# Kernel tuning notes

Measured on AMD Instinct MI355X. Metric: run time of the kernel, lower is better.

Reference implementation:

```python
import jax, jax.numpy as jnp
import numpy as np
import math

D_MODEL = 512
NUM_HEADS = 8
B, S = 2, 4096


def setup_inputs() -> dict:
    key = jax.random.key(0)
    ks = jax.random.split(key, 11)
    d = D_MODEL
    sc = 1.0 / math.sqrt(d)
    return {
        "query": jax.random.normal(ks[0], (B, S, d), jnp.float32),
        "key": jax.random.normal(ks[1], (B, S, d), jnp.float32),
        "value": jax.random.normal(ks[2], (B, S, d), jnp.float32),
        "Wq": jax.random.normal(ks[3], (d, d), jnp.float32) * sc,
        "bq": jnp.zeros((d,), jnp.float32),
        "Wk": jax.random.normal(ks[4], (d, d), jnp.float32) * sc,
        "bk": jnp.zeros((d,), jnp.float32),
        "Wv": jax.random.normal(ks[5], (d, d), jnp.float32) * sc,
        "bv": jnp.zeros((d,), jnp.float32),
        "Wo": jax.random.normal(ks[6], (d, d), jnp.float32) * sc,
        "bo": jnp.zeros((d,), jnp.float32),
    }


def reference(query, key, value, Wq, bq, Wk, bk, Wv, bv, Wo, bo):
    b, q_len, d_model = query.shape
    k_len = key.shape[1]
    h = NUM_HEADS
    d_k = d_model // h
    q = (query @ Wq.T + bq).reshape(b, q_len, h, d_k)
    k = (key @ Wk.T + bk).reshape(b, k_len, h, d_k)
    v = (value @ Wv.T + bv).reshape(b, k_len, h, d_k)
    # NOTE: faithful to source — softmax WITHOUT pre-scaling, then divide by sqrt(d_k)
    comp = jnp.einsum('bqhd,bkhd->bhqk', q, k)
    attn = jax.nn.softmax(comp, axis=-1) / jnp.sqrt(jnp.asarray(d_k, comp.dtype))
    x = jnp.einsum('bhqk,bkhd->bqhd', attn, v)
    return x.reshape(b, q_len, d_model) @ Wo.T + bo
```

## Files before the change

### kernel.cpp

```cpp
#include <hip/hip_runtime.h>

typedef _Float16 f16;
typedef __fp16 fp16x2 __attribute__((ext_vector_type(2)));
typedef _Float16 half4 __attribute__((ext_vector_type(4)));
typedef _Float16 half8 __attribute__((ext_vector_type(8)));
typedef float f32x4 __attribute__((ext_vector_type(4)));
typedef float float4v __attribute__((ext_vector_type(4)));
typedef float float2v __attribute__((ext_vector_type(2)));

#define LOG2E 1.44269504088896340736f

__device__ __forceinline__ half8 cat8(half4 a, half4 b) {
    half8 r;
    r[0] = a[0]; r[1] = a[1]; r[2] = a[2]; r[3] = a[3];
    r[4] = b[0]; r[5] = b[1]; r[6] = b[2]; r[7] = b[3];
    return r;
}

union H8 { fp16x2 h2[4]; half8 h8; };

#define TR8(baddr, d0,d1,d2,d3,d4,d5,d6,d7)                                   \
  asm volatile("ds_read_b64_tr_b16 %0, %8 offset:0\n\t"                       \
               "ds_read_b64_tr_b16 %1, %8 offset:512\n\t"                     \
               "ds_read_b64_tr_b16 %2, %8 offset:128\n\t"                     \
               "ds_read_b64_tr_b16 %3, %8 offset:640\n\t"                     \
               "ds_read_b64_tr_b16 %4, %8 offset:256\n\t"                     \
               "ds_read_b64_tr_b16 %5, %8 offset:768\n\t"                     \
               "ds_read_b64_tr_b16 %6, %8 offset:384\n\t"                     \
               "ds_read_b64_tr_b16 %7, %8 offset:896"                         \
               : "=&v"(d0),"=&v"(d1),"=&v"(d2),"=&v"(d3),                     \
                 "=&v"(d4),"=&v"(d5),"=&v"(d6),"=&v"(d7)                      \
               : "v"(baddr) : "memory")

#define LGKM0_FENCE()                                                          \
  do { asm volatile("s_waitcnt lgkmcnt(0)" ::: "memory");                      \
       __builtin_amdgcn_sched_barrier(0); } while (0)

__device__ __forceinline__ float rowmax16(const f32x4 sf[4]) {
    float a = fmaxf(fmaxf(sf[0][0], sf[0][1]), fmaxf(sf[0][2], sf[0][3]));
    float b = fmaxf(fmaxf(sf[1][0], sf[1][1]), fmaxf(sf[1][2], sf[1][3]));
    float c = fmaxf(fmaxf(sf[2][0], sf[2][1]), fmaxf(sf[2][2], sf[2][3]));
    float d = fmaxf(fmaxf(sf[3][0], sf[3][1]), fmaxf(sf[3][2], sf[3][3]));
    return fmaxf(fmaxf(a, b), fmaxf(c, d));
}

__device__ __forceinline__ void max_defer(
    const f32x4 sf[4], float& mL, f32x4 o[4], f32x4& la)
{
    float vm = rowmax16(sf);
    vm = fmaxf(vm, __shfl_xor(vm, 16, 64));
    vm = fmaxf(vm, __shfl_xor(vm, 32, 64));
    float vmL = vm * LOG2E;
    if (__any(vmL > mL + 8.0f)) {
        float mn = fmaxf(mL, vmL);
        float al = __builtin_amdgcn_exp2f(mL - mn);
        la *= al;
        #pragma unroll
        for (int db = 0; db < 4; ++db) o[db] *= al;
        mL = mn;
    }
}

__device__ __forceinline__ void exp_pack(
    const f32x4 sf[4], float mL, H8& pb0, H8& pb1)
{
    float pe[16];
    #pragma unroll
    for (int kb = 0; kb < 4; ++kb)
        #pragma unroll
        for (int ro = 0; ro < 4; ++ro)
            pe[kb * 4 + ro] = __builtin_amdgcn_exp2f(fmaf(sf[kb][ro], LOG2E, -mL));
    pb0.h2[0] = __builtin_amdgcn_cvt_pkrtz(pe[0],  pe[1]);
    pb0.h2[1] = __builtin_amdgcn_cvt_pkrtz(pe[2],  pe[3]);
    pb0.h2[2] = __builtin_amdgcn_cvt_pkrtz(pe[4],  pe[5]);
    pb0.h2[3] = __builtin_amdgcn_cvt_pkrtz(pe[6],  pe[7]);
    pb1.h2[0] = __builtin_amdgcn_cvt_pkrtz(pe[8],  pe[9]);
    pb1.h2[1] = __builtin_amdgcn_cvt_pkrtz(pe[10], pe[11]);
    pb1.h2[2] = __builtin_amdgcn_cvt_pkrtz(pe[12], pe[13]);
    pb1.h2[3] = __builtin_amdgcn_cvt_pkrtz(pe[14], pe[15]);
}

__global__ __launch_bounds__(256) void qkv_proj(
    const float* __restrict__ Aq, const float* __restrict__ Ak, const float* __restrict__ Av,
    const float* __restrict__ Wq, const float* __restrict__ Wk, const float* __restrict__ Wv,
    const float* __restrict__ bq, const float* __restrict__ bk, const float* __restrict__ bv,
    f16* __restrict__ Qh, f16* __restrict__ Kh, f16* __restrict__ Vh)
{
    const int z = blockIdx.z;
    const float* __restrict__ A    = (z == 0) ? Aq : (z == 1) ? Ak : Av;
    const float* __restrict__ W    = (z == 0) ? Wq : (z == 1) ? Wk : Wv;
    const float* __restrict__ bias = (z == 0) ? bq : (z == 1) ? bk : bv;
    f16* __restrict__ dst          = (z == 0) ? Qh : (z == 1) ? Kh : Vh;

    __shared__ __align__(16) f16 As[128 * 40];
    __shared__ __align__(16) f16 Ws[128 * 40];

    const int t  = threadIdx.x;
    const int m0 = blockIdx.y * 128;
    const int n0 = blockIdx.x * 128;
    const int w = t >> 6, lane = t & 63, lr = lane & 15, lg = lane >> 4;
    const int wr = w >> 1, wc = w & 1;

    f32x4 acc[4][4] = {};

    for (int k0 = 0; k0 < 512; k0 += 32) {
        #pragma unroll
        for (int it = 0; it < 2; ++it) {
            int c = t + it * 256;
            int row  = c >> 2;
            int col8 = (c & 3) * 8;

            const float* ga = A + (size_t)(m0 + row) * 512 + k0 + col8;
            float4v a0 = *(const float4v*)ga;
            float4v a1 = *(const float4v*)(ga + 4);
            half8 ha;
            ha[0] = (f16)a0[0]; ha[1] = (f16)a0[1]; ha[2] = (f16)a0[2]; ha[3] = (f16)a0[3];
            ha[4] = (f16)a1[0]; ha[5] = (f16)a1[1]; ha[6] = (f16)a1[2]; ha[7] = (f16)a1[3];
            *(half8*)&As[row * 40 + col8] = ha;

            const float* gw = W + (size_t)(n0 + row) * 512 + k0 + col8;
            float4v w0 = *(const float4v*)gw;
            float4v w1 = *(const float4v*)(gw + 4);
            half8 hw;
            hw[0] = (f16)w0[0]; hw[1] = (f16)w0[1]; hw[2] = (f16)w0[2]; hw[3] = (f16)w0[3];
            hw[4] = (f16)w1[0]; hw[5] = (f16)w1[1]; hw[6] = (f16)w1[2]; hw[7] = (f16)w1[3];
            *(half8*)&Ws[row * 40 + col8] = hw;
        }
        __syncthreads();

        half8 af[4], bf[4];
        #pragma unroll
        for (int i = 0; i < 4; ++i) {
            af[i] = *(const half8*)&As[(wr * 64 + i * 16 + lr) * 40 + lg * 8];
            bf[i] = *(const half8*)&Ws[(wc * 64 + i * 16 + lr) * 40 + lg * 8];
        }
        #pragma unroll
        for (int mi = 0; mi < 4; ++mi)
            #pragma unroll
            for (int ni = 0; ni < 4; ++ni)
                acc[mi][ni] = __builtin_amdgcn_mfma_f32_16x16x32_f16(af[mi], bf[ni], acc[mi][ni], 0, 0, 0);
        __syncthreads();
    }

    #pragma unroll
    for (int mi = 0; mi < 4; ++mi) {
        #pragma unroll
        for (int ni = 0; ni < 4; ++ni) {
            int col = n0 + wc * 64 + ni * 16 + lr;
            float bv_ = bias[col];
            int h  = col >> 6;
            int dd = col & 63;
            #pragma unroll
            for (int r = 0; r < 4; ++r) {
                int row = m0 + wr * 64 + mi * 16 + lg * 4 + r;
                int b = row >> 12;
                int s = row & 4095;
                dst[(((size_t)(b * 8 + h)) * 4096 + s) * 64 + dd] = (f16)(acc[mi][ni][r] + bv_);
            }
        }
    }
}

__global__ __launch_bounds__(256, 2) void flash_attn(
    const f16* __restrict__ Qh, const f16* __restrict__ Kh, const f16* __restrict__ Vh,
    f16* __restrict__ Xp, float2v* __restrict__ mlp)
{
    const int bh  = blockIdx.y;
    const int z   = blockIdx.z;
    const int t = threadIdx.x, w = t >> 6, lane = t & 63, lr = lane & 15, lg = lane >> 4;
    const int q0 = blockIdx.x * 128 + w * 32;

    __shared__ __align__(16) f16 Ks[2][64 * 72];
    __shared__ __align__(16) f16 Vs[2][64 * 64];

    const size_t hb = (size_t)bh * (4096 * 64);

    half8 aq00 = *(const half8*)&Qh[hb + (size_t)(q0 + lr) * 64 + lg * 8];
    half8 aq01 = *(const half8*)&Qh[hb + (size_t)(q0 + lr) * 64 + 32 + lg * 8];
    half8 aq10 = *(const half8*)&Qh[hb + (size_t)(q0 + 16 + lr) * 64 + lg * 8];
    half8 aq11 = *(const half8*)&Qh[hb + (size_t)(q0 + 16 + lr) * 64 + 32 + lg * 8];

    half8 ones;
    #pragma unroll
    for (int j = 0; j < 8; ++j) ones[j] = (f16)1.0f;
    const f32x4 zf = {0.0f, 0.0f, 0.0f, 0.0f};

    const int srow = t >> 3;
    const int scol = (t & 7) * 8;
    const int kdstA = srow * 72 + scol;
    const int kdstB = kdstA + 32 * 72;
    const int vdstA = ((((srow >> 2) & 3) * 16) + (srow >> 4) * 4 + (scol >> 4)) * 64
                    + (srow & 3) * 16 + (scol & 15);
    const int vdstB = vdstA + 512;

    f32x4 o0[4] = {}, o1[4] = {};
    f32x4 la0 = {}, la1 = {};
    float mL0 = -INFINITY, mL1 = -INFINITY;

    const f16* kbase = Kh + hb + (size_t)(z * 2048 + srow) * 64 + scol;
    const f16* vbase = Vh + hb + (size_t)(z * 2048 + srow) * 64 + scol;

    half8 kregA = *(const half8*)kbase;
    half8 kregB = *(const half8*)(kbase + 2048);
    half8 vregA = *(const half8*)vbase;
    half8 vregB = *(const half8*)(vbase + 2048);

    for (int kt = 0; kt < 2048; kt += 64) {
        const int bi = (kt >> 6) & 1;
        f16* ks = &Ks[bi][0];
        f16* vs = &Vs[bi][0];

        *(half8*)&ks[kdstA] = kregA;
        *(half8*)&ks[kdstB] = kregB;
        *(half8*)&vs[vdstA] = vregA;
        *(half8*)&vs[vdstB] = vregB;
        __syncthreads();

        int koff = ((kt + 64) & 2047) << 6;
        kregA = *(const half8*)(kbase + koff);
        kregB = *(const half8*)(kbase + 2048 + koff);
        vregA = *(const half8*)(vbase + koff);
        vregB = *(const half8*)(vbase + 2048 + koff);

        f32x4 sf0[4], sf1[4];
        {
            half8 kf[4];
            #pragma unroll
            for (int kb = 0; kb < 4; ++kb)
                kf[kb] = *(const half8*)&ks[(kb * 16 + lr) * 72 + lg * 8];
            __builtin_amdgcn_s_setprio(1);
            #pragma unroll
            for (int kb = 0; kb < 4; ++kb)
                sf0[kb] = __builtin_amdgcn_mfma_f32_16x16x32_f16(kf[kb], aq00, zf, 0, 0, 0);
            #pragma unroll
            for (int kb = 0; kb < 4; ++kb)
                sf1[kb] = __builtin_amdgcn_mfma_f32_16x16x32_f16(kf[kb], aq10, zf, 0, 0, 0);
            __builtin_amdgcn_s_setprio(0);
            #pragma unroll
            for (int kb = 0; kb < 4; ++kb)
                kf[kb] = *(const half8*)&ks[(kb * 16 + lr) * 72 + 32 + lg * 8];
            __builtin_amdgcn_s_setprio(1);
            #pragma unroll
            for (int kb = 0; kb < 4; ++kb)
                sf0[kb] = __builtin_amdgcn_mfma_f32_16x16x32_f16(kf[kb], aq01, sf0[kb], 0, 0, 0);
            #pragma unroll
            for (int kb = 0; kb < 4; ++kb)
                sf1[kb] = __builtin_amdgcn_mfma_f32_16x16x32_f16(kf[kb], aq11, sf1[kb], 0, 0, 0);
            __builtin_amdgcn_s_setprio(0);
        }

        max_defer(sf0, mL0, o0, la0);
        max_defer(sf1, mL1, o1, la1);

        const unsigned vb = (unsigned)(size_t)vs + (unsigned)(lg * 2048 + lr * 8);
        half4 ua0,ua1,ua2,ua3,ua4,ua5,ua6,ua7;
        half4 ub0,ub1,ub2,ub3,ub4,ub5,ub6,ub7;
        TR8(vb,         ua0,ua1,ua2,ua3,ua4,ua5,ua6,ua7);
        TR8(vb + 1024u, ub0,ub1,ub2,ub3,ub4,ub5,ub6,ub7);

        H8 p00, p01, p10, p11;
        exp_pack(sf0, mL0, p00, p01);
        exp_pack(sf1, mL1, p10, p11);

        LGKM0_FENCE();

        __builtin_amdgcn_s_setprio(1);
        o0[0] = __builtin_amdgcn_mfma_f32_16x16x32_f16(cat8(ua0,ua1), p00.h8, o0[0], 0, 0, 0);
        o0[1] = __builtin_amdgcn_mfma_f32_16x16x32_f16(cat8(ua2,ua3), p00.h8, o0[1], 0, 0, 0);
        o0[2] = __builtin_amdgcn_mfma_f32_16x16x32_f16(cat8(ua4,ua5), p00.h8, o0[2], 0, 0, 0);
        o0[3] = __builtin_amdgcn_mfma_f32_16x16x32_f16(cat8(ua6,ua7), p00.h8, o0[3], 0, 0, 0);
        o1[0] = __builtin_amdgcn_mfma_f32_16x16x32_f16(cat8(ua0,ua1), p10.h8, o1[0], 0, 0, 0);
        o1[1] = __builtin_amdgcn_mfma_f32_16x16x32_f16(cat8(ua2,ua3), p10.h8, o1[1], 0, 0, 0);
        o1[2] = __builtin_amdgcn_mfma_f32_16x16x32_f16(cat8(ua4,ua5), p10.h8, o1[2], 0, 0, 0);
        o1[3] = __builtin_amdgcn_mfma_f32_16x16x32_f16(cat8(ua6,ua7), p10.h8, o1[3], 0, 0, 0);
        la0 = __builtin_amdgcn_mfma_f32_16x16x32_f16(ones, p00.h8, la0, 0, 0, 0);
        la1 = __builtin_amdgcn_mfma_f32_16x16x32_f16(ones, p10.h8, la1, 0, 0, 0);
        o0[0] = __builtin_amdgcn_mfma_f32_16x16x32_f16(cat8(ub0,ub1), p01.h8, o0[0], 0, 0, 0);
        o0[1] = __builtin_amdgcn_mfma_f32_16x16x32_f16(cat8(ub2,ub3), p01.h8, o0[1], 0, 0, 0);
        o0[2] = __builtin_amdgcn_mfma_f32_16x16x32_f16(cat8(ub4,ub5), p01.h8, o0[2], 0, 0, 0);
        o0[3] = __builtin_amdgcn_mfma_f32_16x16x32_f16(cat8(ub6,ub7), p01.h8, o0[3], 0, 0, 0);
        o1[0] = __builtin_amdgcn_mfma_f32_16x16x32_f16(cat8(ub0,ub1), p11.h8, o1[0], 0, 0, 0);
        o1[1] = __builtin_amdgcn_mfma_f32_16x16x32_f16(cat8(ub2,ub3), p11.h8, o1[1], 0, 0, 0);
        o1[2] = __builtin_amdgcn_mfma_f32_16x16x32_f16(cat8(ub4,ub5), p11.h8, o1[2], 0, 0, 0);
        o1[3] = __builtin_amdgcn_mfma_f32_16x16x32_f16(cat8(ub6,ub7), p11.h8, o1[3], 0, 0, 0);
        la0 = __builtin_amdgcn_mfma_f32_16x16x32_f16(ones, p01.h8, la0, 0, 0, 0);
        la1 = __builtin_amdgcn_mfma_f32_16x16x32_f16(ones, p11.h8, la1, 0, 0, 0);
        __builtin_amdgcn_s_setprio(0);
    }

    const int b = bh >> 3, h = bh & 7;
    f16* X = Xp + (size_t)z * (8192 * 512);
    const float inv0 = 1.0f / la0[0];
    const float inv1 = 1.0f / la1[0];
    const int q0_ = q0 + lr, q1_ = q0 + 16 + lr;
    #pragma unroll
    for (int db = 0; db < 4; ++db) {
        half4 hv0, hv1;
        hv0[0] = (f16)(o0[db][0] * inv0);
        hv0[1] = (f16)(o0[db][1] * inv0);
        hv0[2] = (f16)(o0[db][2] * inv0);
        hv0[3] = (f16)(o0[db][3] * inv0);
        *(half4*)&X[((size_t)(b * 4096 + q0_)) * 512 + h * 64 + db * 16 + lg * 4] = hv0;
        hv1[0] = (f16)(o1[db][0] * inv1);
        hv1[1] = (f16)(o1[db][1] * inv1);
        hv1[2] = (f16)(o1[db][2] * inv1);
        hv1[3] = (f16)(o1[db][3] * inv1);
        *(half4*)&X[((size_t)(b * 4096 + q1_)) * 512 + h * 64 + db * 16 + lg * 4] = hv1;
    }

    if (lane < 16) {
        float2v m0v; m0v[0] = mL0; m0v[1] = la0[0];
        float2v m1v; m1v[0] = mL1; m1v[1] = la1[0];
        mlp[(size_t)z * 65536 + bh * 4096 + q0_] = m0v;
        mlp[(size_t)z * 65536 + bh * 4096 + q1_] = m1v;
    }
}

__global__ __launch_bounds__(256) void combine_halves(
    const f16* __restrict__ Xp, const float2v* __restrict__ mlp,
    f16* __restrict__ Xh)
{
    const size_t idx  = (size_t)blockIdx.x * 256 + threadIdx.x;
    const size_t flat = idx * 8;
    const int h = (int)((flat >> 6) & 7);
    const int s = (int)((flat >> 9) & 4095);
    const int b = (int)(flat >> 21);
    const int bhq = (b * 8 + h) * 4096 + s;

    float2v ml1 = mlp[bhq];
    float2v ml2 = mlp[65536 + bhq];
    float mm = fmaxf(ml1[0], ml2[0]);
    float a1 = __builtin_amdgcn_exp2f(ml1[0] - mm) * ml1[1];
    float a2 = __builtin_amdgcn_exp2f(ml2[0] - mm) * ml2[1];
    float inv = 1.0f / (8.0f * (a1 + a2));
    float w1 = a1 * inv, w2 = a2 * inv;

    half8 x1 = *(const half8*)&Xp[flat];
    half8 x2 = *(const half8*)&Xp[(size_t)8192 * 512 + flat];
    half8 r;
    #pragma unroll
    for (int j = 0; j < 8; ++j)
        r[j] = (f16)(w1 * (float)x1[j] + w2 * (float)x2[j]);
    *(half8*)&Xh[flat] = r;
}

__global__ __launch_bounds__(256) void out_proj(
    const f16* __restrict__ Xh, const float* __restrict__ Wo, const float* __restrict__ bo,
    float* __restrict__ out)
{
    __shared__ __align__(16) f16 As[128 * 40];
    __shared__ __align__(16) f16 Ws[128 * 40];

    const int t  = threadIdx.x;
    const int m0 = blockIdx.y * 128;
    const int n0 = blockIdx.x * 128;
    const int w = t >> 6, lane = t & 63, lr = lane & 15, lg = lane >> 4;
    const int wr = w >> 1, wc = w & 1;

    f32x4 acc[4][4] = {};

    for (int k0 = 0; k0 < 512; k0 += 32) {
        #pragma unroll
        for (int it = 0; it < 2; ++it) {
            int c = t + it * 256;
            int row  = c >> 2;
            int col8 = (c & 3) * 8;

            *(half8*)&As[row * 40 + col8] =
                *(const half8*)&Xh[(size_t)(m0 + row) * 512 + k0 + col8];

            const float* gw = Wo + (size_t)(n0 + row) * 512 + k0 + col8;
            float4v w0 = *(const float4v*)gw;
            float4v w1 = *(const float4v*)(gw + 4);
            half8 hw;
            hw[0] = (f16)w0[0]; hw[1] = (f16)w0[1]; hw[2] = (f16)w0[2]; hw[3] = (f16)w0[3];
            hw[4] = (f16)w1[0]; hw[5] = (f16)w1[1]; hw[6] = (f16)w1[2]; hw[7] = (f16)w1[3];
            *(half8*)&Ws[row * 40 + col8] = hw;
        }
        __syncthreads();

        half8 af[4], bf[4];
        #pragma unroll
        for (int i = 0; i < 4; ++i) {
            af[i] = *(const half8*)&As[(wr * 64 + i * 16 + lr) * 40 + lg * 8];
            bf[i] = *(const half8*)&Ws[(wc * 64 + i * 16 + lr) * 40 + lg * 8];
        }
        #pragma unroll
        for (int mi = 0; mi < 4; ++mi)
            #pragma unroll
            for (int ni = 0; ni < 4; ++ni)
                acc[mi][ni] = __builtin_amdgcn_mfma_f32_16x16x32_f16(af[mi], bf[ni], acc[mi][ni], 0, 0, 0);
        __syncthreads();
    }

    #pragma unroll
    for (int mi = 0; mi < 4; ++mi) {
        #pragma unroll
        for (int ni = 0; ni < 4; ++ni) {
            int col = n0 + wc * 64 + ni * 16 + lr;
            float bb = bo[col];
            #pragma unroll
            for (int r = 0; r < 4; ++r) {
                int row = m0 + wr * 64 + mi * 16 + lg * 4 + r;
                out[(size_t)row * 512 + col] = acc[mi][ni][r] + bb;
            }
        }
    }
}

extern "C" void kernel_launch(void* const* d_in, const int* in_sizes, int n_in,
                              void* d_out, int out_size, void* d_ws, size_t ws_size,
                              hipStream_t stream) {
    const float* query = (const float*)d_in[0];
    const float* key   = (const float*)d_in[1];
    const float* value = (const float*)d_in[2];
    const float* Wq    = (const float*)d_in[3];
    const float* bq    = (const float*)d_in[4];
    const float* Wk    = (const float*)d_in[5];
    const float* bk    = (const float*)d_in[6];
    const float* Wv    = (const float*)d_in[7];
    const float* bv    = (const float*)d_in[8];
    const float* Wo    = (const float*)d_in[9];
    const float* bo    = (const float*)d_in[10];
    float* out = (float*)d_out;

    char* ws = (char*)d_ws;
    f16*     Qh  = (f16*)(ws);
    f16*     Kh  = (f16*)(ws + 8388608);
    f16*     Vh  = (f16*)(ws + 16777216);
    f16*     Xp  = (f16*)(ws + 25165824);
    float2v* mlp = (float2v*)(ws + 41943040);
    f16*     Xh  = (f16*)(ws + 42991616);

    qkv_proj<<<dim3(4, 64, 3), 256, 0, stream>>>(query, key, value,
                                                 Wq, Wk, Wv, bq, bk, bv,
                                                 Qh, Kh, Vh);
    flash_attn<<<dim3(32, 16, 2), 256, 0, stream>>>(Qh, Kh, Vh, Xp, mlp);
    combine_halves<<<2048, 256, 0, stream>>>(Xp, mlp, Xh);
    out_proj<<<dim3(4, 64), 256, 0, stream>>>(Xh, Wo, bo, out);
}
```

Baseline: 166.6 us.

## Fold running max into MFMA accumulator seed and fuse split-K combine into out_proj

Pre-scales Q by log2(e) and seeds the QK^T MFMA accumulator with the negative running max, so the common path computes exp2 directly from the scores without a per-element FMA. The max rescale happens only when a new row max exceeds the threshold. The separate combine_halves kernel is removed and its weighted merge of the two KV-half partials is folded into out_proj's A-tile load. This saves a kernel launch and a global round-trip of Xh. The cost is redundant mlp loads and exp work per out_proj tile (each row is re-merged by the 4 column blocks), plus some fp16 rounding from scaling Q.

```diff
diff --git a/kernel.cpp b/kernel.cpp
--- a/kernel.cpp
+++ b/kernel.cpp
@@ -36,40 +36,44 @@
   do { asm volatile("s_waitcnt lgkmcnt(0)" ::: "memory");                      \
        __builtin_amdgcn_sched_barrier(0); } while (0)
 
-__device__ __forceinline__ float rowmax16(const f32x4 sf[4]) {
-    float a = fmaxf(fmaxf(sf[0][0], sf[0][1]), fmaxf(sf[0][2], sf[0][3]));
-    float b = fmaxf(fmaxf(sf[1][0], sf[1][1]), fmaxf(sf[1][2], sf[1][3]));
-    float c = fmaxf(fmaxf(sf[2][0], sf[2][1]), fmaxf(sf[2][2], sf[2][3]));
-    float d = fmaxf(fmaxf(sf[3][0], sf[3][1]), fmaxf(sf[3][2], sf[3][3]));
-    return fmaxf(fmaxf(a, b), fmaxf(c, d));
-}
-
-__device__ __forceinline__ void max_defer(
-    const f32x4 sf[4], float& mL, f32x4 o[4], f32x4& la)
-{
-    float vm = rowmax16(sf);
-    vm = fmaxf(vm, __shfl_xor(vm, 16, 64));
-    vm = fmaxf(vm, __shfl_xor(vm, 32, 64));
-    float vmL = vm * LOG2E;
-    if (__any(vmL > mL + 8.0f)) {
-        float mn = fmaxf(mL, vmL);
-        float al = __builtin_amdgcn_exp2f(mL - mn);
-        la *= al;
-        #pragma unroll
-        for (int db = 0; db < 4; ++db) o[db] *= al;
-        mL = mn;
-    }
-}
-
-__device__ __forceinline__ void exp_pack(
-    const f32x4 sf[4], float mL, H8& pb0, H8& pb1)
+__device__ __forceinline__ float rowmax16(const f32x4 s[4]) {
+    float p0 = fmaxf(fmaxf(s[0][0], s[0][1]), s[0][2]);
+    float p1 = fmaxf(fmaxf(s[0][3], s[1][0]), s[1][1]);
+    float p2 = fmaxf(fmaxf(s[1][2], s[1][3]), s[2][0]);
+    float p3 = fmaxf(fmaxf(s[2][1], s[2][2]), s[2][3]);
+    float p4 = fmaxf(fmaxf(s[3][0], s[3][1]), s[3][2]);
+    float q0 = fmaxf(fmaxf(p0, p1), p2);
+    float q1 = fmaxf(fmaxf(p3, p4), s[3][3]);
+    return fmaxf(q0, q1);
+}
+
+__device__ __forceinline__ void exp_pack0(const f32x4 sf[4], H8& pb0, H8& pb1)
 {
     float pe[16];
     #pragma unroll
     for (int kb = 0; kb < 4; ++kb)
         #pragma unroll
         for (int ro = 0; ro < 4; ++ro)
-            pe[kb * 4 + ro] = __builtin_amdgcn_exp2f(fmaf(sf[kb][ro], LOG2E, -mL));
+            pe[kb * 4 + ro] = __builtin_amdgcn_exp2f(sf[kb][ro]);
+    pb0.h2[0] = __builtin_amdgcn_cvt_pkrtz(pe[0],  pe[1]);
+    pb0.h2[1] = __builtin_amdgcn_cvt_pkrtz(pe[2],  pe[3]);
+    pb0.h2[2] = __builtin_amdgcn_cvt_pkrtz(pe[4],  pe[5]);
+    pb0.h2[3] = __builtin_amdgcn_cvt_pkrtz(pe[6],  pe[7]);
+    pb1.h2[0] = __builtin_amdgcn_cvt_pkrtz(pe[8],  pe[9]);
+    pb1.h2[1] = __builtin_amdgcn_cvt_pkrtz(pe[10], pe[11]);
+    pb1.h2[2] = __builtin_amdgcn_cvt_pkrtz(pe[12], pe[13]);
+    pb1.h2[3] = __builtin_amdgcn_cvt_pkrtz(pe[14], pe[15]);
+}
+
+__device__ __forceinline__ void exp_pack_sub(const f32x4 sf[4], float vmc,
+                                             H8& pb0, H8& pb1)
+{
+    float pe[16];
+    #pragma unroll
+    for (int kb = 0; kb < 4; ++kb)
+        #pragma unroll
+        for (int ro = 0; ro < 4; ++ro)
+            pe[kb * 4 + ro] = __builtin_amdgcn_exp2f(sf[kb][ro] - vmc);
     pb0.h2[0] = __builtin_amdgcn_cvt_pkrtz(pe[0],  pe[1]);
     pb0.h2[1] = __builtin_amdgcn_cvt_pkrtz(pe[2],  pe[3]);
     pb0.h2[2] = __builtin_amdgcn_cvt_pkrtz(pe[4],  pe[5]);
@@ -179,11 +183,17 @@
     half8 aq01 = *(const half8*)&Qh[hb + (size_t)(q0 + lr) * 64 + 32 + lg * 8];
     half8 aq10 = *(const half8*)&Qh[hb + (size_t)(q0 + 16 + lr) * 64 + lg * 8];
     half8 aq11 = *(const half8*)&Qh[hb + (size_t)(q0 + 16 + lr) * 64 + 32 + lg * 8];
+    #pragma unroll
+    for (int j = 0; j < 8; ++j) {
+        aq00[j] = (f16)((float)aq00[j] * LOG2E);
+        aq01[j] = (f16)((float)aq01[j] * LOG2E);
+        aq10[j] = (f16)((float)aq10[j] * LOG2E);
+        aq11[j] = (f16)((float)aq11[j] * LOG2E);
+    }
 
     half8 ones;
     #pragma unroll
     for (int j = 0; j < 8; ++j) ones[j] = (f16)1.0f;
-    const f32x4 zf = {0.0f, 0.0f, 0.0f, 0.0f};
 
     const int srow = t >> 3;
     const int scol = (t & 7) * 8;
@@ -195,7 +205,8 @@
 
     f32x4 o0[4] = {}, o1[4] = {};
     f32x4 la0 = {}, la1 = {};
-    float mL0 = -INFINITY, mL1 = -INFINITY;
+    f32x4 nseed0 = {}, nseed1 = {};
+    float mL0 = 0.0f, mL1 = 0.0f;
 
     const f16* kbase = Kh + hb + (size_t)(z * 2048 + srow) * 64 + scol;
     const f16* vbase = Vh + hb + (size_t)(z * 2048 + srow) * 64 + scol;
@@ -231,10 +242,10 @@
             __builtin_amdgcn_s_setprio(1);
             #pragma unroll
             for (int kb = 0; kb < 4; ++kb)
-                sf0[kb] = __builtin_amdgcn_mfma_f32_16x16x32_f16(kf[kb], aq00, zf, 0, 0, 0);
-            #pragma unroll
-            for (int kb = 0; kb < 4; ++kb)
-                sf1[kb] = __builtin_amdgcn_mfma_f32_16x16x32_f16(kf[kb], aq10, zf, 0, 0, 0);
+                sf0[kb] = __builtin_amdgcn_mfma_f32_16x16x32_f16(kf[kb], aq00, nseed0, 0, 0, 0);
+            #pragma unroll
+            for (int kb = 0; kb < 4; ++kb)
+                sf1[kb] = __builtin_amdgcn_mfma_f32_16x16x32_f16(kf[kb], aq10, nseed1, 0, 0, 0);
             __builtin_amdgcn_s_setprio(0);
             #pragma unroll
             for (int kb = 0; kb < 4; ++kb)
@@ -249,8 +260,12 @@
             __builtin_amdgcn_s_setprio(0);
         }
 
-        max_defer(sf0, mL0, o0, la0);
-        max_defer(sf1, mL1, o1, la1);
+        float vm0 = rowmax16(sf0);
+        vm0 = fmaxf(vm0, __shfl_xor(vm0, 16, 64));
+        vm0 = fmaxf(vm0, __shfl_xor(vm0, 32, 64));
+        float vm1 = rowmax16(sf1);
+        vm1 = fmaxf(vm1, __shfl_xor(vm1, 16, 64));
+        vm1 = fmaxf(vm1, __shfl_xor(vm1, 32, 64));
 
         const unsigned vb = (unsigned)(size_t)vs + (unsigned)(lg * 2048 + lr * 8);
         half4 ua0,ua1,ua2,ua3,ua4,ua5,ua6,ua7;
@@ -259,8 +274,30 @@
         TR8(vb + 1024u, ub0,ub1,ub2,ub3,ub4,ub5,ub6,ub7);
 
         H8 p00, p01, p10, p11;
-        exp_pack(sf0, mL0, p00, p01);
-        exp_pack(sf1, mL1, p10, p11);
+        if (__any(vm0 > 8.0f)) {
+            float vmc = fmaxf(vm0, 0.0f);
+            float al = __builtin_amdgcn_exp2f(-vmc);
+            la0 *= al;
+            #pragma unroll
+            for (int db = 0; db < 4; ++db) o0[db] *= al;
+            mL0 += vmc;
+            nseed0[0] = -mL0; nseed0[1] = -mL0; nseed0[2] = -mL0; nseed0[3] = -mL0;
+            exp_pack_sub(sf0, vmc, p00, p01);
+        } else {
+            exp_pack0(sf0, p00, p01);
+        }
+        if (__any(vm1 > 8.0f)) {
+            float vmc = fmaxf(vm1, 0.0f);
+            float al = __builtin_amdgcn_exp2f(-vmc);
+            la1 *= al;
+            #pragma unroll
+            for (int db = 0; db < 4; ++db) o1[db] *= al;
+            mL1 += vmc;
+            nseed1[0] = -mL1; nseed1[1] = -mL1; nseed1[2] = -mL1; nseed1[3] = -mL1;
+            exp_pack_sub(sf1, vmc, p10, p11);
+        } else {
+            exp_pack0(sf1, p10, p11);
+        }
 
         LGKM0_FENCE();
 
@@ -316,36 +353,9 @@
     }
 }
 
-__global__ __launch_bounds__(256) void combine_halves(
+__global__ __launch_bounds__(256) void out_proj(
     const f16* __restrict__ Xp, const float2v* __restrict__ mlp,
-    f16* __restrict__ Xh)
-{
-    const size_t idx  = (size_t)blockIdx.x * 256 + threadIdx.x;
-    const size_t flat = idx * 8;
-    const int h = (int)((flat >> 6) & 7);
-    const int s = (int)((flat >> 9) & 4095);
-    const int b = (int)(flat >> 21);
-    const int bhq = (b * 8 + h) * 4096 + s;
-
-    float2v ml1 = mlp[bhq];
-    float2v ml2 = mlp[65536 + bhq];
-    float mm = fmaxf(ml1[0], ml2[0]);
-    float a1 = __builtin_amdgcn_exp2f(ml1[0] - mm) * ml1[1];
-    float a2 = __builtin_amdgcn_exp2f(ml2[0] - mm) * ml2[1];
-    float inv = 1.0f / (8.0f * (a1 + a2));
-    float w1 = a1 * inv, w2 = a2 * inv;
-
-    half8 x1 = *(const half8*)&Xp[flat];
-    half8 x2 = *(const half8*)&Xp[(size_t)8192 * 512 + flat];
-    half8 r;
-    #pragma unroll
-    for (int j = 0; j < 8; ++j)
-        r[j] = (f16)(w1 * (float)x1[j] + w2 * (float)x2[j]);
-    *(half8*)&Xh[flat] = r;
-}
-
-__global__ __launch_bounds__(256) void out_proj(
-    const f16* __restrict__ Xh, const float* __restrict__ Wo, const float* __restrict__ bo,
+    const float* __restrict__ Wo, const float* __restrict__ bo,
     float* __restrict__ out)
 {
     __shared__ __align__(16) f16 As[128 * 40];
@@ -365,16 +375,33 @@
             int c = t + it * 256;
             int row  = c >> 2;
             int col8 = (c & 3) * 8;
-
-            *(half8*)&As[row * 40 + col8] =
-                *(const half8*)&Xh[(size_t)(m0 + row) * 512 + k0 + col8];
+            int gcol = k0 + col8;
+            int tok  = m0 + row;
+
+            int bhq = ((tok >> 12) * 8 + (gcol >> 6)) * 4096 + (tok & 4095);
+            float2v ml1 = mlp[bhq];
+            float2v ml2 = mlp[65536 + bhq];
+            float mm = fmaxf(ml1[0], ml2[0]);
+            float a1 = __builtin_amdgcn_exp2f(ml1[0] - mm) * ml1[1];
+            float a2 = __builtin_amdgcn_exp2f(ml2[0] - mm) * ml2[1];
+            float inv = 1.0f / (8.0f * (a1 + a2));
+            float w1 = a1 * inv, w2 = a2 * inv;
+
+            const size_t xoff = (size_t)tok * 512 + gcol;
+            half8 x1 = *(const half8*)&Xp[xoff];
+            half8 x2 = *(const half8*)&Xp[(size_t)8192 * 512 + xoff];
+            half8 hx;
+            #pragma unroll
+            for (int j = 0; j < 8; ++j)
+                hx[j] = (f16)(w1 * (float)x1[j] + w2 * (float)x2[j]);
+            *(half8*)&As[row * 40 + col8] = hx;
 
             const float* gw = Wo + (size_t)(n0 + row) * 512 + k0 + col8;
             float4v w0 = *(const float4v*)gw;
-            float4v w1 = *(const float4v*)(gw + 4);
+            float4v w1v = *(const float4v*)(gw + 4);
             half8 hw;
-            hw[0] = (f16)w0[0]; hw[1] = (f16)w0[1]; hw[2] = (f16)w0[2]; hw[3] = (f16)w0[3];
-            hw[4] = (f16)w1[0]; hw[5] = (f16)w1[1]; hw[6] = (f16)w1[2]; hw[7] = (f16)w1[3];
+            hw[0] = (f16)w0[0];  hw[1] = (f16)w0[1];  hw[2] = (f16)w0[2];  hw[3] = (f16)w0[3];
+            hw[4] = (f16)w1v[0]; hw[5] = (f16)w1v[1]; hw[6] = (f16)w1v[2]; hw[7] = (f16)w1v[3];
             *(half8*)&Ws[row * 40 + col8] = hw;
         }
         __syncthreads();
@@ -430,12 +457,10 @@
     f16*     Vh  = (f16*)(ws + 16777216);
     f16*     Xp  = (f16*)(ws + 25165824);
     float2v* mlp = (float2v*)(ws + 41943040);
-    f16*     Xh  = (f16*)(ws + 42991616);
 
     qkv_proj<<<dim3(4, 64, 3), 256, 0, stream>>>(query, key, value,
                                                  Wq, Wk, Wv, bq, bk, bv,
                                                  Qh, Kh, Vh);
     flash_attn<<<dim3(32, 16, 2), 256, 0, stream>>>(Qh, Kh, Vh, Xp, mlp);
-    combine_halves<<<2048, 256, 0, stream>>>(Xp, mlp, Xh);
-    out_proj<<<dim3(4, 64), 256, 0, stream>>>(Xh, Wo, bo, out);
-}
+    out_proj<<<dim3(4, 64), 256, 0, stream>>>(Xp, mlp, Wo, bo, out);
+}
```

New measurement: 172.1 us. 1.03x slower.
